# Optimization experiments

Hardware: AMD Instinct MI355X
Metric: run time of the kernel (lower is better)

The kernel has to match this reference:

```python
import jax, jax.numpy as jnp
import numpy as np

N_EMBD = 1024
N_HEAD = 16
HEAD_SIZE = N_EMBD // N_HEAD


def setup_inputs() -> dict:
    key = jax.random.key(0)
    k_x, k_w, k_b = jax.random.split(key, 3)
    B, T, C = 2, 2048, N_EMBD
    x = jax.random.normal(k_x, (B, T, C), dtype=jnp.float32)
    # Linear(n_embd, 3*n_embd): weight [C, 3C] (applied as x @ W), bias [3C]
    w_qkv = jax.random.normal(k_w, (C, 3 * C), dtype=jnp.float32) * (1.0 / np.sqrt(C))
    b_qkv = jax.random.normal(k_b, (3 * C,), dtype=jnp.float32) * 0.02
    return {"x": x, "w_qkv": w_qkv, "b_qkv": b_qkv}


def reference(x, w_qkv, b_qkv):
    B, T, C = x.shape
    H, D = N_HEAD, HEAD_SIZE
    qkv = x @ w_qkv + b_qkv                      # [B, T, 3C]
    q, k, v = jnp.split(qkv, 3, axis=-1)         # each [B, T, C]
    # [B, T, C] -> [B, H, T, D]
    q = q.reshape(B, T, H, D).transpose(0, 2, 1, 3)
    k = k.reshape(B, T, H, D).transpose(0, 2, 1, 3)
    v = v.reshape(B, T, H, D).transpose(0, 2, 1, 3)
    scores = jnp.einsum('bhqd,bhkd->bhqk', q, k) / jnp.sqrt(jnp.float32(D))
    causal = jnp.tril(jnp.ones((T, T), dtype=bool))  # allow j <= i
    scores = jnp.where(causal[None, None, :, :], scores, -jnp.inf)
    weights = jax.nn.softmax(scores, axis=-1)    # [B, H, T, T]
    out = jnp.einsum('bhqk,bhkd->bhqd', weights, v)
    out = out.transpose(0, 2, 1, 3).reshape(B, T, C)
    return out
```

## Files before the change

kernel.cpp:

```cpp
#include <hip/hip_runtime.h>
#include <hip/hip_bf16.h>


#define CDIM  1024
#define C3    3072
#define HS    64
#define TLEN  2048
#define KVT   64
#define SCL   0.1803368801111204f

typedef __attribute__((ext_vector_type(8))) short bf16x8;
typedef __attribute__((ext_vector_type(4))) float f32x4;
typedef __attribute__((ext_vector_type(4))) unsigned short u16x4;

__device__ __forceinline__ unsigned short f2b(float f) {
    unsigned u = __float_as_uint(f);
    unsigned r = (u + 0x7FFFu + ((u >> 16) & 1u)) >> 16;
    return (unsigned short)r;
}
__device__ __forceinline__ float b2f(unsigned short u) {
    return __uint_as_float(((unsigned)u) << 16);
}
__device__ __forceinline__ float fexp2(float x) {
    return __builtin_amdgcn_exp2f(x);
}
__device__ __forceinline__ unsigned pkbf(float a, float b) {
    float2 f; f.x = a; f.y = b;
    __hip_bfloat162 h = __float22bfloat162_rn(f);
    union { __hip_bfloat162 h2; unsigned u; } c;
    c.h2 = h;
    return c.u;
}
__device__ __forceinline__ void gl_lds16(const unsigned short* g, unsigned short* l) {
    __builtin_amdgcn_global_load_lds((const __attribute__((address_space(1))) void*)g,
                                     (__attribute__((address_space(3))) void*)l, 16, 0, 0);
}
__device__ __forceinline__ int detect_bf(const void* bias, int lane) {
    unsigned w = ((const unsigned*)bias)[lane];
    unsigned e = (w >> 7) & 0xFF;
    unsigned long long m = __ballot(e >= 100 && e <= 135);
    return __popcll(m) >= 48;
}

__device__ __forceinline__ void plswap(unsigned x, unsigned& y0, unsigned& y1) {
    unsigned aa = x, bb = x;
    asm("v_permlane32_swap_b32 %0, %1" : "+v"(aa), "+v"(bb));
    asm("v_permlane16_swap_b32 %0, %1" : "+v"(aa), "+v"(bb));
    y0 = aa; y1 = bb;
}
__device__ __forceinline__ bf16x8 xfrag(unsigned x00, unsigned x01,
                                        unsigned x10, unsigned x11, int qsel) {
    unsigned y000, y100, y001, y101, y010, y110, y011, y111;
    plswap(x00, y000, y100);
    plswap(x01, y001, y101);
    plswap(x10, y010, y110);
    plswap(x11, y011, y111);
    union { unsigned u[4]; bf16x8 v; } r;
    r.u[0] = qsel ? y010 : y000;
    r.u[1] = qsel ? y011 : y001;
    r.u[2] = qsel ? y110 : y100;
    r.u[3] = qsel ? y111 : y101;
    return r.v;
}

__global__ __launch_bounds__(256) void k_prep(const void* __restrict__ w,
                                              const void* __restrict__ x,
                                              const void* __restrict__ bias,
                                              unsigned short* __restrict__ wt,
                                              unsigned short* __restrict__ xb) {
    __shared__ unsigned short tile[64 * 66];
    int t = threadIdx.x;
    int isbf = detect_bf(bias, t & 63);
    int bid = blockIdx.x;

    {
        int n0 = (bid % 48) * 64;
        int k0 = (bid / 48) * 64;
        for (int i = 0; i < 16; ++i) {
            int idx = t + i * 256;
            int r = idx >> 6, c = idx & 63;
            unsigned short v;
            if (isbf) v = ((const unsigned short*)w)[(k0 + r) * C3 + n0 + c];
            else      v = f2b(((const float*)w)[(k0 + r) * C3 + n0 + c]);
            tile[r * 66 + c] = v;
        }
        __syncthreads();
        for (int i = 0; i < 16; ++i) {
            int idx = t + i * 256;
            int r = idx >> 6, c = idx & 63;
            wt[(n0 + r) * CDIM + k0 + c] = tile[c * 66 + r];
        }
    }
    if (!isbf) {
        const float* s = (const float*)x;
        unsigned* d = (unsigned*)xb;
        for (int sb = bid; sb < 2048; sb += 768) {
            int base = sb * 1024;
            for (int j = t; j < 1024; j += 256) {
                int idx = base + j;
                float a = s[2 * idx], b = s[2 * idx + 1];
                d[idx] = (unsigned)f2b(a) | ((unsigned)f2b(b) << 16);
            }
        }
    }
}

__global__ __launch_bounds__(256, 3) void k_gemm_qkv(const void* __restrict__ xraw,
                                                     const unsigned short* __restrict__ xb,
                                                     const void* __restrict__ biasraw,
                                                     const unsigned short* __restrict__ Bt,
                                                     unsigned short* __restrict__ qk,
                                                     unsigned short* __restrict__ k2,
                                                     unsigned short* __restrict__ v2) {
    __shared__ __align__(16) unsigned short As[128 * 64];
    __shared__ __align__(16) unsigned short Bs[128 * 64];
    int tid  = threadIdx.x;
    int lane = tid & 63, wv = tid >> 6;
    int quad = lane >> 4, l16 = lane & 15;
    int isbf = detect_bf(biasraw, lane);
    const unsigned short* A = isbf ? (const unsigned short*)xraw : xb;

    int lin = blockIdx.x + 24 * blockIdx.y;
    int swz = (lin & 7) * 96 + (lin >> 3);
    int m0 = (swz / 24) * 128, n0 = (swz % 24) * 128;
    int wm = (wv >> 1) * 64, wn = (wv & 1) * 64;

    f32x4 acc[4][4] = {};

    int srow = wv * 8 + (lane >> 3);
    int kcg8 = (((lane & 7) ^ (lane >> 3)) * 8);
    const unsigned short* Ag = A  + (m0 + srow) * CDIM + kcg8;
    const unsigned short* Bg = Bt + (n0 + srow) * CDIM + kcg8;
    unsigned short* lA = &As[srow * 64 + (lane & 7) * 8];
    unsigned short* lB = &Bs[srow * 64 + (lane & 7) * 8];

    for (int k0 = 0; k0 < CDIM; k0 += 64) {
        __syncthreads();
        for (int j = 0; j < 4; ++j) {
            gl_lds16(Ag + j * (32 * CDIM), lA + j * (32 * 64));
            gl_lds16(Bg + j * (32 * CDIM), lB + j * (32 * 64));
        }
        Ag += 64; Bg += 64;
        __syncthreads();

        for (int kk = 0; kk < 2; ++kk) {
            int sw = (l16 & 7);
            bf16x8 af[4], bfr[4];
            for (int mt = 0; mt < 4; ++mt)
                af[mt] = *(const bf16x8*)&As[(wm + mt * 16 + l16) * 64 + (((kk * 4 + quad) ^ sw) * 8)];
            for (int nt = 0; nt < 4; ++nt)
                bfr[nt] = *(const bf16x8*)&Bs[(wn + nt * 16 + l16) * 64 + (((kk * 4 + quad) ^ sw) * 8)];
            for (int mt = 0; mt < 4; ++mt)
                for (int nt = 0; nt < 4; ++nt)
                    acc[mt][nt] = __builtin_amdgcn_mfma_f32_16x16x32_bf16(af[mt], bfr[nt], acc[mt][nt], 0, 0, 0);
        }
    }

    if (n0 < 1024) {
        for (int mt = 0; mt < 4; ++mt) {
            int row = m0 + wm + mt * 16 + quad * 4;
            for (int nt = 0; nt < 4; ++nt) {
                int col = n0 + wn + nt * 16 + l16;
                float bv = isbf ? b2f(((const unsigned short*)biasraw)[col])
                                : ((const float*)biasraw)[col];
                for (int i = 0; i < 4; ++i)
                    qk[(row + i) * 2048 + col] = f2b(acc[mt][nt][i] + bv);
            }
        }
    } else if (n0 < 2048) {
        for (int mt = 0; mt < 4; ++mt) {
            int row = m0 + wm + mt * 16 + quad * 4;
            int tq = row & 2047, b = row >> 11;
            for (int nt = 0; nt < 4; ++nt) {
                int col = n0 + wn + nt * 16 + l16;
                float bv = isbf ? b2f(((const unsigned short*)biasraw)[col])
                                : ((const float*)biasraw)[col];
                int c = col - 1024;
                int hh = c >> 6, d = c & 63;
                int base = ((b * 16 + hh) * 32 + (tq >> 6)) * 4096
                         + ((tq >> 5) & 1) * 2048 + ((tq >> 4) & 1) * 1024
                         + (d >> 5) * 512 + ((d >> 3) & 3) * 128
                         + (tq & 15) * 8 + (d & 7);
                for (int i = 0; i < 4; ++i)
                    k2[base + i * 8] = f2b(acc[mt][nt][i] + bv);
            }
        }
    } else {
        for (int mt = 0; mt < 4; ++mt) {
            int row = m0 + wm + mt * 16 + quad * 4;
            int tq = row & 2047, b = row >> 11;
            for (int nt = 0; nt < 4; ++nt) {
                int col = n0 + wn + nt * 16 + l16;
                float bv = isbf ? b2f(((const unsigned short*)biasraw)[col])
                                : ((const float*)biasraw)[col];
                int c = col - 2048;
                int hh = c >> 6, d = c & 63;
                int base = ((b * 16 + hh) * 32 + (tq >> 6)) * 4096
                         + ((tq >> 5) & 1) * 2048 + (d >> 4) * 512
                         + ((tq >> 3) & 3) * 128 + (d & 15) * 8 + (tq & 7);
                u16x4 pk;
                for (int i = 0; i < 4; ++i) pk[i] = f2b(acc[mt][nt][i] + bv);
                *(u16x4*)&v2[base] = pk;
            }
        }
    }
}

__global__ __launch_bounds__(256, 4) void k_attn(const unsigned short* __restrict__ qk,
                                                 const unsigned short* __restrict__ k2,
                                                 const unsigned short* __restrict__ v2,
                                                 const void* __restrict__ biasraw,
                                                 void* __restrict__ outv) {
    __shared__ __align__(16) float SMf[4416];

    int tid  = threadIdx.x;
    int lane = tid & 63, wv = tid >> 6;
    int quad = lane >> 4, l16 = lane & 15;
    int isbf = detect_bf(biasraw, lane);
    int bh = blockIdx.x;
    int g  = 31 - blockIdx.y;
    int b = bh >> 4, h = bh & 15;
    int rowbase = b * TLEN;

    int s_ = wv >> 1;
    int p  = wv & 1;
    int qbase = 64 * g + 32 * s_;
    int T  = g + 1;
    int Tw = T - ((s_ == 0 && p == 1) ? 1 : 0);
    bool dmw = (p == s_);

    bf16x8 qf[2][2];
    for (int qt = 0; qt < 2; ++qt)
        for (int kh = 0; kh < 2; ++kh)
            qf[qt][kh] = *(const bf16x8*)&qk[(rowbase + qbase + qt * 16 + l16) * 2048
                                            + h * HS + kh * 32 + quad * 8];

    f32x4 o[2][4] = {};
    float ls[2] = {0.f, 0.f};

    const unsigned short* kp = k2 + bh * 131072 + p * 2048 + lane * 8;
    const unsigned short* vp = v2 + bh * 131072 + p * 2048 + lane * 8;

    bf16x8 kf00, kf01, kf10, kf11;
    if (Tw > 0) {
        kf00 = *(const bf16x8*)kp;
        kf01 = *(const bf16x8*)(kp + 512);
        kf10 = *(const bf16x8*)(kp + 1024);
        kf11 = *(const bf16x8*)(kp + 1536);
        kp += 4096;
    }

    for (int t = 0; t < Tw; ++t) {
        bf16x8 av0 = *(const bf16x8*)vp;
        bf16x8 av1 = *(const bf16x8*)(vp + 512);
        bf16x8 av2 = *(const bf16x8*)(vp + 1024);
        bf16x8 av3 = *(const bf16x8*)(vp + 1536);
        vp += 4096;

        f32x4 sv[2][2];
        __builtin_amdgcn_s_setprio(1);
        #pragma unroll
        for (int qt = 0; qt < 2; ++qt) {
            f32x4 z0 = {};
            z0 = __builtin_amdgcn_mfma_f32_16x16x32_bf16(kf00, qf[qt][0], z0, 0, 0, 0);
            z0 = __builtin_amdgcn_mfma_f32_16x16x32_bf16(kf01, qf[qt][1], z0, 0, 0, 0);
            sv[qt][0] = z0;
            f32x4 z1 = {};
            z1 = __builtin_amdgcn_mfma_f32_16x16x32_bf16(kf10, qf[qt][0], z1, 0, 0, 0);
            z1 = __builtin_amdgcn_mfma_f32_16x16x32_bf16(kf11, qf[qt][1], z1, 0, 0, 0);
            sv[qt][1] = z1;
        }
        __builtin_amdgcn_s_setprio(0);

        bool pf = (t + 1 < Tw);
        bf16x8 kn00 = *(const bf16x8*)kp;
        bf16x8 kn01 = *(const bf16x8*)(kp + 512);
        bf16x8 kn10 = *(const bf16x8*)(kp + 1024);
        bf16x8 kn11 = *(const bf16x8*)(kp + 1536);
        kp += 4096;

        unsigned sp[2][2][2];
        int kvb = t * KVT + 32 * p;
        if (dmw && (t == T - 1)) {
            #pragma unroll
            for (int qt = 0; qt < 2; ++qt) {
                float psum = 0.f;
                int q = qbase + qt * 16 + l16;
                #pragma unroll
                for (int nt = 0; nt < 2; ++nt) {
                    float pv[4];
                    #pragma unroll
                    for (int i = 0; i < 4; ++i) {
                        float arg = fmaf(sv[qt][nt][i], SCL, -12.0f);
                        int kv = kvb + nt * 16 + quad * 4 + i;
                        if (kv > q) arg = -1e30f;
                        pv[i] = fexp2(arg);
                        psum += pv[i];
                    }
                    sp[qt][nt][0] = pkbf(pv[0], pv[1]);
                    sp[qt][nt][1] = pkbf(pv[2], pv[3]);
                }
                ls[qt] += psum;
            }
        } else {
            #pragma unroll
            for (int qt = 0; qt < 2; ++qt) {
                float psum = 0.f;
                #pragma unroll
                for (int nt = 0; nt < 2; ++nt) {
                    float pv[4];
                    #pragma unroll
                    for (int i = 0; i < 4; ++i) {
                        float arg = fmaf(sv[qt][nt][i], SCL, -12.0f);
                        pv[i] = fexp2(arg);
                        psum += pv[i];
                    }
                    sp[qt][nt][0] = pkbf(pv[0], pv[1]);
                    sp[qt][nt][1] = pkbf(pv[2], pv[3]);
                }
                ls[qt] += psum;
            }
        }

        int qsel = quad & 2;
        bf16x8 f0 = xfrag(sp[0][0][0], sp[0][0][1], sp[0][1][0], sp[0][1][1], qsel);
        bf16x8 f1 = xfrag(sp[1][0][0], sp[1][0][1], sp[1][1][0], sp[1][1][1], qsel);
        __builtin_amdgcn_s_setprio(1);
        o[0][0] = __builtin_amdgcn_mfma_f32_16x16x32_bf16(av0, f0, o[0][0], 0, 0, 0);
        o[1][0] = __builtin_amdgcn_mfma_f32_16x16x32_bf16(av0, f1, o[1][0], 0, 0, 0);
        o[0][1] = __builtin_amdgcn_mfma_f32_16x16x32_bf16(av1, f0, o[0][1], 0, 0, 0);
        o[1][1] = __builtin_amdgcn_mfma_f32_16x16x32_bf16(av1, f1, o[1][1], 0, 0, 0);
        o[0][2] = __builtin_amdgcn_mfma_f32_16x16x32_bf16(av2, f0, o[0][2], 0, 0, 0);
        o[1][2] = __builtin_amdgcn_mfma_f32_16x16x32_bf16(av2, f1, o[1][2], 0, 0, 0);
        o[0][3] = __builtin_amdgcn_mfma_f32_16x16x32_bf16(av3, f0, o[0][3], 0, 0, 0);
        o[1][3] = __builtin_amdgcn_mfma_f32_16x16x32_bf16(av3, f1, o[1][3], 0, 0, 0);
        __builtin_amdgcn_s_setprio(0);

        if (pf) { kf00 = kn00; kf01 = kn01; kf10 = kn10; kf11 = kn11; }
    }

    #pragma unroll
    for (int qt = 0; qt < 2; ++qt) {
        ls[qt] += __shfl_xor(ls[qt], 16);
        ls[qt] += __shfl_xor(ls[qt], 32);
    }
    float* mrg  = SMf;
    float* lbuf = SMf + 4352;

    if (p == 1) {
        #pragma unroll
        for (int qt = 0; qt < 2; ++qt)
            #pragma unroll
            for (int dt = 0; dt < 4; ++dt)
                *(f32x4*)&mrg[s_ * (32 * 68) + (qt * 16 + l16) * 68 + dt * 16 + quad * 4] = o[qt][dt];
        if (quad == 0) {
            lbuf[s_ * 32 + l16]      = ls[0];
            lbuf[s_ * 32 + 16 + l16] = ls[1];
        }
    }
    __syncthreads();
    if (p == 0) {
        #pragma unroll
        for (int qt = 0; qt < 2; ++qt) {
            float lt = ls[qt] + lbuf[s_ * 32 + qt * 16 + l16];
            float inv = 1.0f / lt;
            int q = qbase + qt * 16 + l16;
            if (isbf) {
                unsigned short* out = (unsigned short*)outv;
                #pragma unroll
                for (int dt = 0; dt < 4; ++dt) {
                    f32x4 m = *(const f32x4*)&mrg[s_ * (32 * 68) + (qt * 16 + l16) * 68 + dt * 16 + quad * 4];
                    u16x4 ov;
                    #pragma unroll
                    for (int i = 0; i < 4; ++i) ov[i] = f2b((o[qt][dt][i] + m[i]) * inv);
                    *(u16x4*)&out[(rowbase + q) * CDIM + h * HS + dt * 16 + quad * 4] = ov;
                }
            } else {
                float* out = (float*)outv;
                #pragma unroll
                for (int dt = 0; dt < 4; ++dt) {
                    f32x4 m = *(const f32x4*)&mrg[s_ * (32 * 68) + (qt * 16 + l16) * 68 + dt * 16 + quad * 4];
                    float4 ov;
                    ov.x = (o[qt][dt][0] + m[0]) * inv;
                    ov.y = (o[qt][dt][1] + m[1]) * inv;
                    ov.z = (o[qt][dt][2] + m[2]) * inv;
                    ov.w = (o[qt][dt][3] + m[3]) * inv;
                    *(float4*)&out[(rowbase + q) * CDIM + h * HS + dt * 16 + quad * 4] = ov;
                }
            }
        }
    }
}

extern "C" void kernel_launch(void* const* d_in, const int* in_sizes, int n_in,
                              void* d_out, int out_size, void* d_ws, size_t ws_size,
                              hipStream_t stream) {
    const void* x    = d_in[0];
    const void* w    = d_in[1];
    const void* bias = d_in[2];

    char* ws = (char*)d_ws;
    unsigned short* xb  = (unsigned short*)ws;
    unsigned short* wt  = (unsigned short*)(ws + (8u  << 20));
    unsigned short* qk  = (unsigned short*)(ws + (16u << 20));
    unsigned short* k2  = (unsigned short*)(ws + (32u << 20));
    unsigned short* v2  = (unsigned short*)(ws + (40u << 20));

    k_prep<<<768, 256, 0, stream>>>(w, x, bias, wt, xb);
    k_gemm_qkv<<<dim3(24, 32), 256, 0, stream>>>(x, xb, bias, wt, qk, k2, v2);
    k_attn<<<dim3(32, 32), 256, 0, stream>>>(qk, k2, v2, bias, d_out);
}
```

Baseline: 149.5 us.

## Restructure QKV GEMM into 256x256 tiles with double-buffered async LDS loads

```diff
diff --git a/kernel.cpp b/kernel.cpp
--- a/kernel.cpp
+++ b/kernel.cpp
@@ -105,62 +105,99 @@
     }
 }
 
-__global__ __launch_bounds__(256, 3) void k_gemm_qkv(const void* __restrict__ xraw,
+__global__ __launch_bounds__(512, 2) void k_gemm_qkv(const void* __restrict__ xraw,
                                                      const unsigned short* __restrict__ xb,
                                                      const void* __restrict__ biasraw,
                                                      const unsigned short* __restrict__ Bt,
                                                      unsigned short* __restrict__ qk,
                                                      unsigned short* __restrict__ k2,
                                                      unsigned short* __restrict__ v2) {
-    __shared__ __align__(16) unsigned short As[128 * 64];
-    __shared__ __align__(16) unsigned short Bs[128 * 64];
+    __shared__ __align__(16) unsigned short As[2 * 256 * 32];
+    __shared__ __align__(16) unsigned short Bs[2 * 256 * 32];
     int tid  = threadIdx.x;
     int lane = tid & 63, wv = tid >> 6;
     int quad = lane >> 4, l16 = lane & 15;
     int isbf = detect_bf(biasraw, lane);
     const unsigned short* A = isbf ? (const unsigned short*)xraw : xb;
 
-    int lin = blockIdx.x + 24 * blockIdx.y;
-    int swz = (lin & 7) * 96 + (lin >> 3);
-    int m0 = (swz / 24) * 128, n0 = (swz % 24) * 128;
-    int wm = (wv >> 1) * 64, wn = (wv & 1) * 64;
-
-    f32x4 acc[4][4] = {};
-
-    int srow = wv * 8 + (lane >> 3);
-    int kcg8 = (((lane & 7) ^ (lane >> 3)) * 8);
-    const unsigned short* Ag = A  + (m0 + srow) * CDIM + kcg8;
-    const unsigned short* Bg = Bt + (n0 + srow) * CDIM + kcg8;
-    unsigned short* lA = &As[srow * 64 + (lane & 7) * 8];
-    unsigned short* lB = &Bs[srow * 64 + (lane & 7) * 8];
-
-    for (int k0 = 0; k0 < CDIM; k0 += 64) {
-        __syncthreads();
-        for (int j = 0; j < 4; ++j) {
-            gl_lds16(Ag + j * (32 * CDIM), lA + j * (32 * 64));
-            gl_lds16(Bg + j * (32 * CDIM), lB + j * (32 * 64));
-        }
-        Ag += 64; Bg += 64;
-        __syncthreads();
-
-        for (int kk = 0; kk < 2; ++kk) {
-            int sw = (l16 & 7);
-            bf16x8 af[4], bfr[4];
-            for (int mt = 0; mt < 4; ++mt)
-                af[mt] = *(const bf16x8*)&As[(wm + mt * 16 + l16) * 64 + (((kk * 4 + quad) ^ sw) * 8)];
+    int lin = blockIdx.x;
+    int swz = (lin & 7) * 24 + (lin >> 3);
+    int m0 = (swz / 12) * 256, n0 = (swz % 12) * 256;
+    int wr = wv >> 2, wc = wv & 3;
+
+    f32x4 acc[8][4] = {};
+
+    int ci0 = tid,        r0 = ci0 >> 2, g0 = ((ci0 & 3) ^ (r0 & 3)) * 8;
+    int ci1 = tid + 512,  r1 = ci1 >> 2, g1 = ((ci1 & 3) ^ (r1 & 3)) * 8;
+    const unsigned short* a0 = A  + (m0 + r0) * CDIM + g0;
+    const unsigned short* a1 = A  + (m0 + r1) * CDIM + g1;
+    const unsigned short* b0 = Bt + (n0 + r0) * CDIM + g0;
+    const unsigned short* b1 = Bt + (n0 + r1) * CDIM + g1;
+    unsigned short* dA0 = As + ci0 * 8;
+    unsigned short* dA1 = As + ci1 * 8;
+    unsigned short* dB0 = Bs + ci0 * 8;
+    unsigned short* dB1 = Bs + ci1 * 8;
+
+    int sw4 = l16 & 3;
+    int aro = (wr * 128 + l16) * 32 + ((quad ^ sw4) * 8);
+    int bro = (wc * 64  + l16) * 32 + ((quad ^ sw4) * 8);
+
+    {
+        gl_lds16(a0,       &As[0 * 8192] + ci0 * 8 - (As - As));
+        gl_lds16(a1,       dA1);
+        gl_lds16(b0,       dB0);
+        gl_lds16(b1,       dB1);
+        gl_lds16(a0 + 32,  dA0 + 8192);
+        gl_lds16(a1 + 32,  dA1 + 8192);
+        gl_lds16(b0 + 32,  dB0 + 8192);
+        gl_lds16(b1 + 32,  dB1 + 8192);
+    }
+    asm volatile("s_waitcnt vmcnt(4)" ::: "memory");
+    __builtin_amdgcn_s_barrier();
+
+    #pragma unroll 2
+    for (int kt = 0; kt < 32; ++kt) {
+        int cur = kt & 1;
+        const unsigned short* Ac = As + cur * 8192;
+        const unsigned short* Bc = Bs + cur * 8192;
+
+        bf16x8 af[8], bfv[4];
+        #pragma unroll
+        for (int mt = 0; mt < 8; ++mt)
+            af[mt] = *(const bf16x8*)&Ac[aro + mt * 512];
+        #pragma unroll
+        for (int nt = 0; nt < 4; ++nt)
+            bfv[nt] = *(const bf16x8*)&Bc[bro + nt * 512];
+
+        __builtin_amdgcn_s_setprio(1);
+        #pragma unroll
+        for (int mt = 0; mt < 8; ++mt)
+            #pragma unroll
             for (int nt = 0; nt < 4; ++nt)
-                bfr[nt] = *(const bf16x8*)&Bs[(wn + nt * 16 + l16) * 64 + (((kk * 4 + quad) ^ sw) * 8)];
-            for (int mt = 0; mt < 4; ++mt)
-                for (int nt = 0; nt < 4; ++nt)
-                    acc[mt][nt] = __builtin_amdgcn_mfma_f32_16x16x32_bf16(af[mt], bfr[nt], acc[mt][nt], 0, 0, 0);
-        }
+                acc[mt][nt] = __builtin_amdgcn_mfma_f32_16x16x32_bf16(af[mt], bfv[nt], acc[mt][nt], 0, 0, 0);
+        __builtin_amdgcn_s_setprio(0);
+
+        __builtin_amdgcn_s_barrier();
+        if (kt < 30) {
+            int koff = (kt + 2) * 32;
+            unsigned short* tA = As + cur * 8192;
+            unsigned short* tB = Bs + cur * 8192;
+            gl_lds16(a0 + koff, tA + ci0 * 8);
+            gl_lds16(a1 + koff, tA + ci1 * 8);
+            gl_lds16(b0 + koff, tB + ci0 * 8);
+            gl_lds16(b1 + koff, tB + ci1 * 8);
+            asm volatile("s_waitcnt vmcnt(4)" ::: "memory");
+        } else {
+            asm volatile("s_waitcnt vmcnt(0)" ::: "memory");
+        }
+        __builtin_amdgcn_s_barrier();
     }
 
     if (n0 < 1024) {
-        for (int mt = 0; mt < 4; ++mt) {
-            int row = m0 + wm + mt * 16 + quad * 4;
+        for (int mt = 0; mt < 8; ++mt) {
+            int row = m0 + wr * 128 + mt * 16 + quad * 4;
             for (int nt = 0; nt < 4; ++nt) {
-                int col = n0 + wn + nt * 16 + l16;
+                int col = n0 + wc * 64 + nt * 16 + l16;
                 float bv = isbf ? b2f(((const unsigned short*)biasraw)[col])
                                 : ((const float*)biasraw)[col];
                 for (int i = 0; i < 4; ++i)
@@ -168,11 +205,11 @@
             }
         }
     } else if (n0 < 2048) {
-        for (int mt = 0; mt < 4; ++mt) {
-            int row = m0 + wm + mt * 16 + quad * 4;
+        for (int mt = 0; mt < 8; ++mt) {
+            int row = m0 + wr * 128 + mt * 16 + quad * 4;
             int tq = row & 2047, b = row >> 11;
             for (int nt = 0; nt < 4; ++nt) {
-                int col = n0 + wn + nt * 16 + l16;
+                int col = n0 + wc * 64 + nt * 16 + l16;
                 float bv = isbf ? b2f(((const unsigned short*)biasraw)[col])
                                 : ((const float*)biasraw)[col];
                 int c = col - 1024;
@@ -186,11 +223,11 @@
             }
         }
     } else {
-        for (int mt = 0; mt < 4; ++mt) {
-            int row = m0 + wm + mt * 16 + quad * 4;
+        for (int mt = 0; mt < 8; ++mt) {
+            int row = m0 + wr * 128 + mt * 16 + quad * 4;
             int tq = row & 2047, b = row >> 11;
             for (int nt = 0; nt < 4; ++nt) {
-                int col = n0 + wn + nt * 16 + l16;
+                int col = n0 + wc * 64 + nt * 16 + l16;
                 float bv = isbf ? b2f(((const unsigned short*)biasraw)[col])
                                 : ((const float*)biasraw)[col];
                 int c = col - 2048;
@@ -407,6 +444,6 @@
     unsigned short* v2  = (unsigned short*)(ws + (40u << 20));
 
     k_prep<<<768, 256, 0, stream>>>(w, x, bias, wt, xb);
-    k_gemm_qkv<<<dim3(24, 32), 256, 0, stream>>>(x, xb, bias, wt, qk, k2, v2);
+    k_gemm_qkv<<<192, 512, 0, stream>>>(x, xb, bias, wt, qk, k2, v2);
     k_attn<<<dim3(32, 32), 256, 0, stream>>>(qk, k2, v2, bias, d_out);
 }
```

New measurement: 158.7 us. 1.06x slower.

## Double-buffer QKV GEMM LDS tiles with async prefetch and MFMA priority

Applied to the files above, without the earlier changes.

```diff
diff --git a/kernel.cpp b/kernel.cpp
--- a/kernel.cpp
+++ b/kernel.cpp
@@ -112,8 +112,8 @@
                                                      unsigned short* __restrict__ qk,
                                                      unsigned short* __restrict__ k2,
                                                      unsigned short* __restrict__ v2) {
-    __shared__ __align__(16) unsigned short As[128 * 64];
-    __shared__ __align__(16) unsigned short Bs[128 * 64];
+    __shared__ __align__(16) unsigned short As[2 * 128 * 32];
+    __shared__ __align__(16) unsigned short Bs[2 * 128 * 32];
     int tid  = threadIdx.x;
     int lane = tid & 63, wv = tid >> 6;
     int quad = lane >> 4, l16 = lane & 15;
@@ -127,33 +127,64 @@
 
     f32x4 acc[4][4] = {};
 
-    int srow = wv * 8 + (lane >> 3);
-    int kcg8 = (((lane & 7) ^ (lane >> 3)) * 8);
-    const unsigned short* Ag = A  + (m0 + srow) * CDIM + kcg8;
-    const unsigned short* Bg = Bt + (n0 + srow) * CDIM + kcg8;
-    unsigned short* lA = &As[srow * 64 + (lane & 7) * 8];
-    unsigned short* lB = &Bs[srow * 64 + (lane & 7) * 8];
-
-    for (int k0 = 0; k0 < CDIM; k0 += 64) {
-        __syncthreads();
-        for (int j = 0; j < 4; ++j) {
-            gl_lds16(Ag + j * (32 * CDIM), lA + j * (32 * 64));
-            gl_lds16(Bg + j * (32 * CDIM), lB + j * (32 * 64));
-        }
-        Ag += 64; Bg += 64;
-        __syncthreads();
-
-        for (int kk = 0; kk < 2; ++kk) {
-            int sw = (l16 & 7);
-            bf16x8 af[4], bfr[4];
-            for (int mt = 0; mt < 4; ++mt)
-                af[mt] = *(const bf16x8*)&As[(wm + mt * 16 + l16) * 64 + (((kk * 4 + quad) ^ sw) * 8)];
+    int r0 = tid >> 2;
+    int g0 = (((tid & 3) ^ (r0 & 3)) * 8);
+    const unsigned short* a0 = A  + (m0 + r0) * CDIM + g0;
+    const unsigned short* b0 = Bt + (n0 + r0) * CDIM + g0;
+    unsigned short* dA = As + tid * 8;
+    unsigned short* dB = Bs + tid * 8;
+
+    int sw4 = l16 & 3;
+    int aro = (wm + l16) * 32 + ((quad ^ sw4) * 8);
+    int bro = (wn + l16) * 32 + ((quad ^ sw4) * 8);
+
+    gl_lds16(a0,                 dA);
+    gl_lds16(a0 + 64 * CDIM,     dA + 2048);
+    gl_lds16(b0,                 dB);
+    gl_lds16(b0 + 64 * CDIM,     dB + 2048);
+    gl_lds16(a0 + 32,            dA + 4096);
+    gl_lds16(a0 + 64 * CDIM + 32, dA + 4096 + 2048);
+    gl_lds16(b0 + 32,            dB + 4096);
+    gl_lds16(b0 + 64 * CDIM + 32, dB + 4096 + 2048);
+    asm volatile("s_waitcnt vmcnt(4)" ::: "memory");
+    __builtin_amdgcn_s_barrier();
+
+    #pragma unroll 2
+    for (int kt = 0; kt < 32; ++kt) {
+        int cur = kt & 1;
+        const unsigned short* Ac = As + cur * 4096;
+        const unsigned short* Bc = Bs + cur * 4096;
+
+        bf16x8 af[4], bfv[4];
+        #pragma unroll
+        for (int mt = 0; mt < 4; ++mt)
+            af[mt] = *(const bf16x8*)&Ac[aro + mt * 512];
+        #pragma unroll
+        for (int nt = 0; nt < 4; ++nt)
+            bfv[nt] = *(const bf16x8*)&Bc[bro + nt * 512];
+
+        __builtin_amdgcn_s_setprio(1);
+        #pragma unroll
+        for (int mt = 0; mt < 4; ++mt)
+            #pragma unroll
             for (int nt = 0; nt < 4; ++nt)
-                bfr[nt] = *(const bf16x8*)&Bs[(wn + nt * 16 + l16) * 64 + (((kk * 4 + quad) ^ sw) * 8)];
-            for (int mt = 0; mt < 4; ++mt)
-                for (int nt = 0; nt < 4; ++nt)
-                    acc[mt][nt] = __builtin_amdgcn_mfma_f32_16x16x32_bf16(af[mt], bfr[nt], acc[mt][nt], 0, 0, 0);
-        }
+                acc[mt][nt] = __builtin_amdgcn_mfma_f32_16x16x32_bf16(af[mt], bfv[nt], acc[mt][nt], 0, 0, 0);
+        __builtin_amdgcn_s_setprio(0);
+
+        __builtin_amdgcn_s_barrier();
+        if (kt < 30) {
+            int koff = (kt + 2) * 32;
+            unsigned short* tA = As + cur * 4096;
+            unsigned short* tB = Bs + cur * 4096;
+            gl_lds16(a0 + koff,            tA + tid * 8);
+            gl_lds16(a0 + 64 * CDIM + koff, tA + tid * 8 + 2048);
+            gl_lds16(b0 + koff,            tB + tid * 8);
+            gl_lds16(b0 + 64 * CDIM + koff, tB + tid * 8 + 2048);
+            asm volatile("s_waitcnt vmcnt(4)" ::: "memory");
+        } else {
+            asm volatile("s_waitcnt vmcnt(0)" ::: "memory");
+        }
+        __builtin_amdgcn_s_barrier();
     }
 
     if (n0 < 1024) {
```

Result: no change. 150.9 us (+1.0%).
